# Kernel tuning notes

Hardware: AMD Instinct MI355X
Metric: run time of the kernel (lower is better)

Reference implementation:

```python
import jax, jax.numpy as jnp
import numpy as np

N_NODES = 100000
N_EDGES = 600000
DIMS = [128, 64, 32, 2]


def gcn_conv(x, edge_index, W, b, n_nodes):
    """PyG GCNConv (eval mode): symmetric-normalized aggregation with self-loops.
    out = D^{-1/2} (A + I) D^{-1/2} (x W) + b
    """
    h = x @ W  # [N, out] -- transform first (cheaper when out < in)
    src = jnp.concatenate([edge_index[0], jnp.arange(n_nodes)])  # add self-loops
    dst = jnp.concatenate([edge_index[1], jnp.arange(n_nodes)])
    deg = jax.ops.segment_sum(jnp.ones_like(dst, dtype=h.dtype), dst,
                              num_segments=n_nodes)  # in-degree incl. self-loop
    dinv = jax.lax.rsqrt(deg)
    norm = dinv[src] * dinv[dst]  # [E+N]
    msg = norm[:, None] * h[src]  # gather + scale
    out = jax.ops.segment_sum(msg, dst, num_segments=n_nodes)  # scatter-add
    return out + b


def setup_inputs() -> dict:
    key = jax.random.key(0)
    ks = jax.random.split(key, 8)
    x = jax.random.normal(ks[0], (N_NODES, DIMS[0]), dtype=jnp.float32)
    edge_index = jax.random.randint(ks[1], (2, N_EDGES), 0, N_NODES, dtype=jnp.int64)
    inp = {"x": x, "edge_index": edge_index}
    for i in range(3):
        fan_in, fan_out = DIMS[i], DIMS[i + 1]
        s = 1.0 / np.sqrt(fan_in)
        inp[f"W{i+1}"] = jax.random.uniform(ks[2 + 2 * i], (fan_in, fan_out),
                                            minval=-s, maxval=s, dtype=jnp.float32)
        inp[f"b{i+1}"] = jnp.zeros((fan_out,), dtype=jnp.float32)
    return inp


def reference(x, edge_index, W1, b1, W2, b2, W3, b3):
    # 3 stacked GCNConv layers with ReLU; dropout is identity in eval mode.
    n = x.shape[0]
    x = jax.nn.relu(gcn_conv(x, edge_index, W1, b1, n))
    x = jax.nn.relu(gcn_conv(x, edge_index, W2, b2, n))
    x = jax.nn.relu(gcn_conv(x, edge_index, W3, b3, n))
    return x
```

## Files before the change

### kernel.cpp

```cpp
#include <hip/hip_runtime.h>
#include <math.h>


#define FULL_GRID 2048

typedef const __attribute__((address_space(1))) void* gas_ptr;
typedef __attribute__((address_space(3))) void* las_ptr;

__device__ __forceinline__ void gld16(const void* g, void* l) {
  __builtin_amdgcn_global_load_lds((gas_ptr)g, (las_ptr)l, 16, 0, 0);
}

__global__ __launch_bounds__(256) void k_detect(const unsigned int* __restrict__ words,
                                                int* __restrict__ flag) {
  __shared__ int sm[256];
  int cnt = 0;
  #pragma unroll
  for (int j = 0; j < 8; ++j) {
    int idx = (threadIdx.x * 8 + j) * 2 + 1;
    cnt += (words[idx] == 0u) ? 1 : 0;
  }
  sm[threadIdx.x] = cnt;
  __syncthreads();
  for (int off = 128; off > 0; off >>= 1) {
    if (threadIdx.x < off) sm[threadIdx.x] += sm[threadIdx.x + off];
    __syncthreads();
  }
  if (threadIdx.x == 0) flag[0] = (sm[0] > 1024) ? 1 : 0;
}

__global__ __launch_bounds__(256) void k_hist(const void* __restrict__ eraw, int E,
                                              const int* __restrict__ flag,
                                              int* __restrict__ counts) {
  const int is64 = flag[0];
  int i = blockIdx.x * blockDim.x + threadIdx.x;
  const int stride = gridDim.x * blockDim.x;
  if (is64) {
    const long long* e = (const long long*)eraw;
    for (; i < E; i += stride) atomicAdd(&counts[(int)e[(long long)E + i]], 1);
  } else {
    const int* e = (const int*)eraw;
    for (; i < E; i += stride) atomicAdd(&counts[e[E + i]], 1);
  }
}

__global__ __launch_bounds__(1024) void k_scan1(const int* __restrict__ counts,
                                                int* __restrict__ scanned,
                                                int* __restrict__ partials, int n) {
  __shared__ int sm[1024];
  const int i = blockIdx.x * 1024 + threadIdx.x;
  const int v = (i < n) ? counts[i] : 0;
  sm[threadIdx.x] = v;
  __syncthreads();
  for (int off = 1; off < 1024; off <<= 1) {
    int t = sm[threadIdx.x];
    int u = (threadIdx.x >= off) ? sm[threadIdx.x - off] : 0;
    __syncthreads();
    sm[threadIdx.x] = t + u;
    __syncthreads();
  }
  const int inc = sm[threadIdx.x];
  if (i < n) scanned[i] = inc - v;
  if (threadIdx.x == 1023) partials[blockIdx.x] = inc;
}

__global__ __launch_bounds__(1024) void k_scan2(int* __restrict__ partials, int nb) {
  __shared__ int sm[1024];
  const int v = (threadIdx.x < nb) ? partials[threadIdx.x] : 0;
  sm[threadIdx.x] = v;
  __syncthreads();
  for (int off = 1; off < 1024; off <<= 1) {
    int t = sm[threadIdx.x];
    int u = (threadIdx.x >= off) ? sm[threadIdx.x - off] : 0;
    __syncthreads();
    sm[threadIdx.x] = t + u;
    __syncthreads();
  }
  if (threadIdx.x < nb) partials[threadIdx.x] = sm[threadIdx.x] - v;
}

__global__ __launch_bounds__(256) void k_scan3(const int* __restrict__ scanned,
                                               const int* __restrict__ partials,
                                               const int* __restrict__ counts,
                                               int* __restrict__ offsets,
                                               int* __restrict__ cursor,
                                               float* __restrict__ dinv, int n) {
  int i = blockIdx.x * blockDim.x + threadIdx.x;
  const int stride = gridDim.x * blockDim.x;
  for (; i < n; i += stride) {
    const int o = scanned[i] + partials[i >> 10];
    offsets[i] = o;
    cursor[i] = o;
    dinv[i] = rsqrtf((float)counts[i] + 1.0f);
  }
}

__global__ __launch_bounds__(256) void k_fill(const void* __restrict__ eraw, int E,
                                              const int* __restrict__ flag,
                                              int* __restrict__ cursor,
                                              int* __restrict__ elist) {
  const int is64 = flag[0];
  int i = blockIdx.x * blockDim.x + threadIdx.x;
  const int stride = gridDim.x * blockDim.x;
  if (is64) {
    const long long* e = (const long long*)eraw;
    for (; i < E; i += stride) {
      const int s = (int)e[i];
      const int d = (int)e[(long long)E + i];
      elist[atomicAdd(&cursor[d], 1)] = s;
    }
  } else {
    const int* e = (const int*)eraw;
    for (; i < E; i += stride) {
      const int s = e[i];
      const int d = e[E + i];
      elist[atomicAdd(&cursor[d], 1)] = s;
    }
  }
}

template <int F_IN, int F_OUT, int TILE_M, int KC>
__global__ __launch_bounds__(256) void k_transform(const float* __restrict__ X,
                                                   const float* __restrict__ W,
                                                   const float* __restrict__ dinv,
                                                   float* __restrict__ H, int n) {
  constexpr int COLT = F_OUT / 4;
  constexpr int ROWT = 256 / COLT;
  constexpr int TM = TILE_M / ROWT;
  constexpr int NKC = F_IN / KC;
  static_assert(TM * ROWT == TILE_M && COLT * 4 == F_OUT, "tiling");
  static_assert((TILE_M * F_IN * 4) % 1024 == 0 && (KC * F_OUT * 4) % 1024 == 0, "segs");

  __shared__ __align__(16) float Xs[TILE_M * F_IN];
  __shared__ __align__(16) float Ws[KC * F_OUT];

  const int tid = threadIdx.x;
  const int lane = tid & 63;
  const int wid = tid >> 6;
  const long long base = (long long)blockIdx.x * TILE_M;

  if (base + TILE_M <= n) {
    constexpr int SEGS = TILE_M * F_IN * 4 / 1024;
    constexpr int PW = SEGS / 4;
    const float* gbase = X + base * F_IN;
    #pragma unroll
    for (int j = 0; j < PW; ++j) {
      const int seg = wid * PW + j;
      gld16(gbase + seg * 256 + lane * 4, &Xs[seg * 256]);
    }
  } else {
    const float4* __restrict__ X4 = (const float4*)X;
    for (int g = tid; g < TILE_M * F_IN / 4; g += 256) {
      const int row = g / (F_IN / 4), c4 = g % (F_IN / 4);
      float4 v = make_float4(0.f, 0.f, 0.f, 0.f);
      if (base + row < n) v = X4[(base + row) * (F_IN / 4) + c4];
      ((float4*)Xs)[g] = v;
    }
  }

  const int ct = tid % COLT;
  const int rt = tid / COLT;

  float4 acc[TM];
  #pragma unroll
  for (int r = 0; r < TM; ++r) acc[r] = make_float4(0.f, 0.f, 0.f, 0.f);

  const float4* Xs4 = (const float4*)Xs;
  const float4* Ws4 = (const float4*)Ws;

  for (int kc = 0; kc < NKC; ++kc) {
    __syncthreads();
    {
      constexpr int WSEG = KC * F_OUT * 4 / 1024;
      constexpr int WPW = WSEG / 4;
      const float* wb = W + kc * KC * F_OUT;
      #pragma unroll
      for (int j = 0; j < WPW; ++j) {
        const int seg = wid * WPW + j;
        gld16(wb + seg * 256 + lane * 4, &Ws[seg * 256]);
      }
    }
    __syncthreads();
    #pragma unroll
    for (int k4 = 0; k4 < KC / 4; ++k4) {
      float4 wv0 = Ws4[(k4 * 4 + 0) * COLT + ct];
      float4 wv1 = Ws4[(k4 * 4 + 1) * COLT + ct];
      float4 wv2 = Ws4[(k4 * 4 + 2) * COLT + ct];
      float4 wv3 = Ws4[(k4 * 4 + 3) * COLT + ct];
      #pragma unroll
      for (int r = 0; r < TM; ++r) {
        const float4 xv = Xs4[(rt + r * ROWT) * (F_IN / 4) + kc * (KC / 4) + k4];
        acc[r].x = fmaf(xv.x, wv0.x, acc[r].x);
        acc[r].y = fmaf(xv.x, wv0.y, acc[r].y);
        acc[r].z = fmaf(xv.x, wv0.z, acc[r].z);
        acc[r].w = fmaf(xv.x, wv0.w, acc[r].w);
        acc[r].x = fmaf(xv.y, wv1.x, acc[r].x);
        acc[r].y = fmaf(xv.y, wv1.y, acc[r].y);
        acc[r].z = fmaf(xv.y, wv1.z, acc[r].z);
        acc[r].w = fmaf(xv.y, wv1.w, acc[r].w);
        acc[r].x = fmaf(xv.z, wv2.x, acc[r].x);
        acc[r].y = fmaf(xv.z, wv2.y, acc[r].y);
        acc[r].z = fmaf(xv.z, wv2.z, acc[r].z);
        acc[r].w = fmaf(xv.z, wv2.w, acc[r].w);
        acc[r].x = fmaf(xv.w, wv3.x, acc[r].x);
        acc[r].y = fmaf(xv.w, wv3.y, acc[r].y);
        acc[r].z = fmaf(xv.w, wv3.z, acc[r].z);
        acc[r].w = fmaf(xv.w, wv3.w, acc[r].w);
      }
    }
  }

  #pragma unroll
  for (int r = 0; r < TM; ++r) {
    const long long row = base + rt + r * ROWT;
    if (row < n) {
      const float di = dinv[row];
      float4 v = acc[r];
      v.x *= di; v.y *= di; v.z *= di; v.w *= di;
      *(float4*)&H[row * F_OUT + ct * 4] = v;
    }
  }
}

template <int F, bool RELU_OUT, bool FUSE_W3>
__global__ __launch_bounds__(256) void k_aggregate(const float* __restrict__ HS,
                                                   const float* __restrict__ dinv,
                                                   const int* __restrict__ offsets,
                                                   const int* __restrict__ counts,
                                                   const int* __restrict__ elist,
                                                   const float* __restrict__ bias,
                                                   const float* __restrict__ W3,
                                                   float* __restrict__ out, int n) {
  const int f = threadIdx.x % F;
  const int grp = threadIdx.x / F;
  constexpr int GRPS = 256 / F;
  const float bf = bias[f];
  float w30 = 0.f, w31 = 0.f;
  if (FUSE_W3) { w30 = W3[f * 2 + 0]; w31 = W3[f * 2 + 1]; }

  for (long long d = (long long)blockIdx.x * GRPS + grp; d < n;
       d += (long long)gridDim.x * GRPS) {
    const float di = dinv[d];
    float acc = HS[d * F + f];
    const int start = offsets[d];
    const int cnt = counts[d];
    for (int j = 0; j < cnt; j += 8) {
      int idx[8];
      float v[8];
      #pragma unroll
      for (int t = 0; t < 8; ++t) {
        const int jj = (j + t < cnt) ? (j + t) : j;
        idx[t] = elist[start + jj];
      }
      #pragma unroll
      for (int t = 0; t < 8; ++t) v[t] = HS[(long long)idx[t] * F + f];
      #pragma unroll
      for (int t = 0; t < 8; ++t) acc += (j + t < cnt) ? v[t] : 0.f;
    }

    float r = fmaf(di, acc, bf);
    if (RELU_OUT) r = fmaxf(r, 0.f);
    if (!FUSE_W3) {
      out[d * F + f] = r;
    } else {
      float t0 = r * w30, t1 = r * w31;
      #pragma unroll
      for (int m = 1; m < 32; m <<= 1) {
        t0 += __shfl_xor(t0, m, 64);
        t1 += __shfl_xor(t1, m, 64);
      }
      if (f == 0) {
        out[d * 2 + 0] = di * t0;
        out[d * 2 + 1] = di * t1;
      }
    }
  }
}

extern "C" void kernel_launch(void* const* d_in, const int* in_sizes, int n_in,
                              void* d_out, int out_size, void* d_ws, size_t ws_size,
                              hipStream_t stream) {
  const float* x = (const float*)d_in[0];
  const void* eraw = d_in[1];
  const float* W1 = (const float*)d_in[2];
  const float* b1 = (const float*)d_in[3];
  const float* W2 = (const float*)d_in[4];
  const float* b2 = (const float*)d_in[5];
  const float* W3 = (const float*)d_in[6];
  const float* b3 = (const float*)d_in[7];
  float* out = (float*)d_out;

  const int N = in_sizes[0] / 128;
  const int E = in_sizes[1] / 2;

  char* ws = (char*)d_ws;
  size_t off = 0;
  auto alloc = [&](size_t bytes) -> char* {
    char* p = ws + off;
    off = (off + bytes + 255) & ~(size_t)255;
    return p;
  };
  int*   flag     = (int*)alloc(256);
  int*   counts   = (int*)alloc((size_t)N * 4);
  int*   scanned  = (int*)alloc((size_t)N * 4);
  int*   partials = (int*)alloc(1024 * 4);
  int*   offsets  = (int*)alloc((size_t)N * 4);
  int*   cursor   = (int*)alloc((size_t)N * 4);
  int*   elist    = (int*)alloc((size_t)E * 4);
  float* dinv     = (float*)alloc((size_t)N * 4);
  float* hbuf     = (float*)alloc((size_t)N * 64 * 4);
  float* obuf     = (float*)alloc((size_t)N * 64 * 4);
  float* h2buf    = (float*)alloc((size_t)N * 32 * 4);
  (void)ws_size; (void)n_in; (void)out_size;

  hipMemsetAsync(counts, 0, (size_t)N * 4, stream);
  k_detect<<<1, 256, 0, stream>>>((const unsigned int*)eraw, flag);
  k_hist<<<FULL_GRID, 256, 0, stream>>>(eraw, E, flag, counts);
  const int NB = (N + 1023) >> 10;
  k_scan1<<<NB, 1024, 0, stream>>>(counts, scanned, partials, N);
  k_scan2<<<1, 1024, 0, stream>>>(partials, NB);
  k_scan3<<<(N + 255) / 256, 256, 0, stream>>>(scanned, partials, counts, offsets,
                                               cursor, dinv, N);
  k_fill<<<FULL_GRID, 256, 0, stream>>>(eraw, E, flag, cursor, elist);

  k_transform<128, 64, 64, 32><<<(N + 63) / 64, 256, 0, stream>>>(x, W1, dinv, hbuf, N);
  k_aggregate<64, true, false><<<(N + 3) / 4, 256, 0, stream>>>(
      hbuf, dinv, offsets, counts, elist, b1, nullptr, obuf, N);

  k_transform<64, 32, 128, 64><<<(N + 127) / 128, 256, 0, stream>>>(obuf, W2, dinv,
                                                                    h2buf, N);
  k_aggregate<32, true, true><<<(N + 7) / 8, 256, 0, stream>>>(
      h2buf, dinv, offsets, counts, elist, b2, W3, hbuf, N);

  k_aggregate<2, true, false><<<(N + 127) / 128, 256, 0, stream>>>(
      hbuf, dinv, offsets, counts, elist, b3, nullptr, out, N);
}
```

Measured before the change: 207.0 us.

## Swizzle X tile in LDS, double-buffer W chunks, replace memset with kernel

The transform kernel now stores the X tile in LDS with an XOR swizzle on the float4 column index, keyed by row. This is meant to avoid LDS bank conflicts when threads read different rows at the same k. W chunks are double-buffered and prefetched one step ahead, which drops one barrier per k-chunk, and the first layer's K chunk shrinks from 32 to 16. The hipMemsetAsync of the counts array is replaced by a small custom zeroing kernel, with the allocation padded for int4 stores. The cost is extra index arithmetic and an extra W buffer in LDS.

```diff
diff --git a/kernel.cpp b/kernel.cpp
--- a/kernel.cpp
+++ b/kernel.cpp
@@ -9,6 +9,13 @@
 
 __device__ __forceinline__ void gld16(const void* g, void* l) {
   __builtin_amdgcn_global_load_lds((gas_ptr)g, (las_ptr)l, 16, 0, 0);
+}
+
+__global__ __launch_bounds__(256) void k_zero(int* __restrict__ p, int n4) {
+  int i = blockIdx.x * blockDim.x + threadIdx.x;
+  const int stride = gridDim.x * blockDim.x;
+  int4* p4 = (int4*)p;
+  for (; i < n4; i += stride) p4[i] = make_int4(0, 0, 0, 0);
 }
 
 __global__ __launch_bounds__(256) void k_detect(const unsigned int* __restrict__ words,
@@ -128,68 +135,84 @@
   constexpr int ROWT = 256 / COLT;
   constexpr int TM = TILE_M / ROWT;
   constexpr int NKC = F_IN / KC;
+  constexpr int K4 = F_IN / 4;
+  constexpr int NWB = (NKC > 1) ? 2 : 1;
   static_assert(TM * ROWT == TILE_M && COLT * 4 == F_OUT, "tiling");
   static_assert((TILE_M * F_IN * 4) % 1024 == 0 && (KC * F_OUT * 4) % 1024 == 0, "segs");
+  static_assert(K4 >= 8, "swizzle range");
 
   __shared__ __align__(16) float Xs[TILE_M * F_IN];
-  __shared__ __align__(16) float Ws[KC * F_OUT];
+  __shared__ __align__(16) float Ws[NWB][KC * F_OUT];
 
   const int tid = threadIdx.x;
   const int lane = tid & 63;
   const int wid = tid >> 6;
   const long long base = (long long)blockIdx.x * TILE_M;
 
+  const float4* __restrict__ X4 = (const float4*)X;
   if (base + TILE_M <= n) {
     constexpr int SEGS = TILE_M * F_IN * 4 / 1024;
     constexpr int PW = SEGS / 4;
-    const float* gbase = X + base * F_IN;
     #pragma unroll
     for (int j = 0; j < PW; ++j) {
       const int seg = wid * PW + j;
-      gld16(gbase + seg * 256 + lane * 4, &Xs[seg * 256]);
+      const int slot = seg * 64 + lane;
+      const int row = slot / K4;
+      const int c = slot % K4;
+      const int ksrc = c ^ (row & 7);
+      gld16(&X4[(base + row) * K4 + ksrc], &Xs[seg * 256]);
     }
   } else {
-    const float4* __restrict__ X4 = (const float4*)X;
-    for (int g = tid; g < TILE_M * F_IN / 4; g += 256) {
-      const int row = g / (F_IN / 4), c4 = g % (F_IN / 4);
+    for (int slot = tid; slot < TILE_M * K4; slot += 256) {
+      const int row = slot / K4;
+      const int c = slot % K4;
       float4 v = make_float4(0.f, 0.f, 0.f, 0.f);
-      if (base + row < n) v = X4[(base + row) * (F_IN / 4) + c4];
-      ((float4*)Xs)[g] = v;
+      if (base + row < n) v = X4[(base + row) * K4 + (c ^ (row & 7))];
+      ((float4*)Xs)[slot] = v;
+    }
+  }
+
+  constexpr int WSEG = KC * F_OUT * 4 / 1024;
+  constexpr int WPW = WSEG / 4;
+  {
+    #pragma unroll
+    for (int j = 0; j < WPW; ++j) {
+      const int seg = wid * WPW + j;
+      gld16(W + seg * 256 + lane * 4, &Ws[0][seg * 256]);
     }
   }
 
   const int ct = tid % COLT;
   const int rt = tid / COLT;
+  const int sw = rt & 7;
 
   float4 acc[TM];
   #pragma unroll
   for (int r = 0; r < TM; ++r) acc[r] = make_float4(0.f, 0.f, 0.f, 0.f);
 
   const float4* Xs4 = (const float4*)Xs;
-  const float4* Ws4 = (const float4*)Ws;
 
   for (int kc = 0; kc < NKC; ++kc) {
     __syncthreads();
-    {
-      constexpr int WSEG = KC * F_OUT * 4 / 1024;
-      constexpr int WPW = WSEG / 4;
-      const float* wb = W + kc * KC * F_OUT;
+    if (NKC > 1 && kc + 1 < NKC) {
+      const float* wb = W + (kc + 1) * KC * F_OUT;
       #pragma unroll
       for (int j = 0; j < WPW; ++j) {
         const int seg = wid * WPW + j;
-        gld16(wb + seg * 256 + lane * 4, &Ws[seg * 256]);
-      }
-    }
-    __syncthreads();
+        gld16(wb + seg * 256 + lane * 4, &Ws[(kc + 1) & (NWB - 1)][seg * 256]);
+      }
+    }
+    const float4* Ws4 = (const float4*)Ws[kc & (NWB - 1)];
     #pragma unroll
     for (int k4 = 0; k4 < KC / 4; ++k4) {
+      const int kk = kc * (KC / 4) + k4;
       float4 wv0 = Ws4[(k4 * 4 + 0) * COLT + ct];
       float4 wv1 = Ws4[(k4 * 4 + 1) * COLT + ct];
       float4 wv2 = Ws4[(k4 * 4 + 2) * COLT + ct];
       float4 wv3 = Ws4[(k4 * 4 + 3) * COLT + ct];
       #pragma unroll
       for (int r = 0; r < TM; ++r) {
-        const float4 xv = Xs4[(rt + r * ROWT) * (F_IN / 4) + kc * (KC / 4) + k4];
+        const float4 xv = Xs4[(rt + r * ROWT) * K4 + (kk ^ sw)];
         acc[r].x = fmaf(xv.x, wv0.x, acc[r].x);
         acc[r].y = fmaf(xv.x, wv0.y, acc[r].y);
         acc[r].z = fmaf(xv.x, wv0.z, acc[r].z);
@@ -301,7 +324,7 @@
     return p;
   };
   int*   flag     = (int*)alloc(256);
-  int*   counts   = (int*)alloc((size_t)N * 4);
+  int*   counts   = (int*)alloc((size_t)N * 4 + 16);
   int*   scanned  = (int*)alloc((size_t)N * 4);
   int*   partials = (int*)alloc(1024 * 4);
   int*   offsets  = (int*)alloc((size_t)N * 4);
@@ -313,7 +336,7 @@
   float* h2buf    = (float*)alloc((size_t)N * 32 * 4);
   (void)ws_size; (void)n_in; (void)out_size;
 
-  hipMemsetAsync(counts, 0, (size_t)N * 4, stream);
+  k_zero<<<128, 256, 0, stream>>>(counts, (N + 3) / 4);
   k_detect<<<1, 256, 0, stream>>>((const unsigned int*)eraw, flag);
   k_hist<<<FULL_GRID, 256, 0, stream>>>(eraw, E, flag, counts);
   const int NB = (N + 1023) >> 10;
@@ -323,7 +346,7 @@
                                                cursor, dinv, N);
   k_fill<<<FULL_GRID, 256, 0, stream>>>(eraw, E, flag, cursor, elist);
 
-  k_transform<128, 64, 64, 32><<<(N + 63) / 64, 256, 0, stream>>>(x, W1, dinv, hbuf, N);
+  k_transform<128, 64, 64, 16><<<(N + 63) / 64, 256, 0, stream>>>(x, W1, dinv, hbuf, N);
   k_aggregate<64, true, false><<<(N + 3) / 4, 256, 0, stream>>>(
       hbuf, dinv, offsets, counts, elist, b1, nullptr, obuf, N);
 
```

New measurement: 202.0 us. 1.02x faster.
